# Performance work log

Measured on AMD Instinct MI355X. Metric: run time of the kernel, lower is better.

The kernel has to match this reference:

```python
import jax, jax.numpy as jnp
import numpy as np

B, D = 256, 1024
EPS = 1e-6


def setup_inputs() -> dict:
    key = jax.random.key(0)
    ks = jax.random.split(key, 8)
    s = 1.0 / np.sqrt(D)
    return {
        "x": jax.random.normal(ks[0], (B, D), jnp.float32),
        "Wq": jax.random.normal(ks[1], (D, D), jnp.float32) * s,
        "bq": jax.random.normal(ks[2], (D,), jnp.float32) * 0.01,
        "Wk": jax.random.normal(ks[3], (D, D), jnp.float32) * s,
        "bk": jax.random.normal(ks[4], (D,), jnp.float32) * 0.01,
        "Wv": jax.random.normal(ks[5], (D, D), jnp.float32) * s,
        "bv": jax.random.normal(ks[6], (D,), jnp.float32) * 0.01,
        "scale": jnp.asarray(1.0, jnp.float32),
        "norm_w": jnp.ones((D,), jnp.float32),
    }


def reference(x, Wq, bq, Wk, bk, Wv, bv, scale, norm_w):
    # QKV projections (torch Linear: x @ W.T + b)
    Q = x @ Wq.T + bq  # [B, D]
    K = x @ Wk.T + bk  # [B, D]
    V = x @ Wv.T + bv  # [B, D]
    # outer-product scores [B, D, D]: scores[b,i,j] = Q[b,i]*K[b,j]/scale
    scores = (Q[:, :, None] * K[:, None, :]) / scale
    attn = jax.nn.softmax(scores, axis=-1)  # [B, D, D]
    attended = jnp.einsum("bij,bj->bi", attn, V)  # [B, D]
    # dropout is identity in eval mode
    h = attended + x
    rms = jnp.sqrt(jnp.mean(h * h, axis=-1, keepdims=True) + EPS)
    return (h / rms) * norm_w
```

## Files before the change

kernel.cpp:

```cpp
#include <hip/hip_runtime.h>
#include <hip/hip_bf16.h>

#define BB 256
#define DD 1024

typedef unsigned short u16;
typedef unsigned int   u32;
typedef __attribute__((ext_vector_type(8))) __bf16 bf16x8;
typedef __attribute__((ext_vector_type(4))) float  floatx4;

__device__ __forceinline__ float bf2f(u16 u) {
    union { u32 i; float f; } t; t.i = ((u32)u) << 16; return t.f;
}
__device__ __forceinline__ u16 f2bf_rne(float f) {
    u32 u = __float_as_uint(f);
    u32 r = u + 0x7FFFu + ((u >> 16) & 1u);
    return (u16)(r >> 16);
}
__device__ __forceinline__ bool detect_bf16(const void* p) {
    return (*(const u32*)p) == 0x3F803F80u;
}
__device__ __forceinline__ float loadf(const void* p, int i, bool bf) {
    return bf ? bf2f(((const u16*)p)[i]) : ((const float*)p)[i];
}

__device__ __forceinline__ float wave_sum64(float x) {
    x += __int_as_float(__builtin_amdgcn_update_dpp(0, __float_as_int(x), 0x111, 0xF, 0xF, true));
    x += __int_as_float(__builtin_amdgcn_update_dpp(0, __float_as_int(x), 0x112, 0xF, 0xF, true));
    x += __int_as_float(__builtin_amdgcn_update_dpp(0, __float_as_int(x), 0x114, 0xF, 0xF, true));
    x += __int_as_float(__builtin_amdgcn_update_dpp(0, __float_as_int(x), 0x118, 0xF, 0xF, true));
    x += __int_as_float(__builtin_amdgcn_update_dpp(0, __float_as_int(x), 0x142, 0xA, 0xF, true));
    x += __int_as_float(__builtin_amdgcn_update_dpp(0, __float_as_int(x), 0x143, 0xC, 0xF, true));
    return x;
}

__device__ __forceinline__ void split1(float f, u16& h, u16& l) {
    u32 u  = __float_as_uint(f);
    u32 hu = u & 0xFFFF0000u;
    h = (u16)(hu >> 16);
    l = f2bf_rne(f - __uint_as_float(hu));
}

__global__ __launch_bounds__(256) void qkv_gemm(
    const void* __restrict__ x,
    const void* __restrict__ Wq, const void* __restrict__ bq,
    const void* __restrict__ Wk, const void* __restrict__ bk,
    const void* __restrict__ Wv, const void* __restrict__ bv,
    const void* __restrict__ nw,
    float* __restrict__ qkv)
{
    const bool bf = detect_bf16(nw);
    const int z = blockIdx.z;
    const void* W    = (z == 0) ? Wq : (z == 1) ? Wk : Wv;
    const void* bias = (z == 0) ? bq : (z == 1) ? bk : bv;
    float* outp = qkv + (size_t)z * BB * DD;

    const int m0 = blockIdx.x * 32;
    const int n0 = blockIdx.y * 64;
    const int tid  = threadIdx.x;
    const int lane = tid & 63;
    const int wave = tid >> 6;
    const int wr = wave & 1, wc = wave >> 1;
    const int l15 = lane & 15, quad = lane >> 4;

    __shared__ __align__(16) u16 Ah[32][72], Al[32][72];
    __shared__ __align__(16) u16 Bh[64][72], Bl[64][72];

    const int arow = tid >> 4;
    const int acol = (tid & 15) * 4;

    floatx4 acc[2] = {(floatx4){0.f,0.f,0.f,0.f}, (floatx4){0.f,0.f,0.f,0.f}};

    float4 ar[2], br[4];
    auto ld4 = [&](const void* p, int idx) -> float4 {
        if (!bf) return *(const float4*)((const float*)p + idx);
        const u16* q = (const u16*)p + idx;
        return make_float4(bf2f(q[0]), bf2f(q[1]), bf2f(q[2]), bf2f(q[3]));
    };
    auto fetch = [&](int k0) {
        #pragma unroll
        for (int f = 0; f < 2; ++f) ar[f] = ld4(x, (m0 + arow + f * 16) * DD + k0 + acol);
        #pragma unroll
        for (int f = 0; f < 4; ++f) br[f] = ld4(W, (n0 + arow + f * 16) * DD + k0 + acol);
    };

    fetch(0);
    for (int k0 = 0; k0 < DD; k0 += 64) {
        #pragma unroll
        for (int f = 0; f < 2; ++f) {
            const int r = arow + f * 16;
            ushort4 h, l;
            split1(ar[f].x, h.x, l.x); split1(ar[f].y, h.y, l.y);
            split1(ar[f].z, h.z, l.z); split1(ar[f].w, h.w, l.w);
            *(ushort4*)&Ah[r][acol] = h;
            *(ushort4*)&Al[r][acol] = l;
        }
        #pragma unroll
        for (int f = 0; f < 4; ++f) {
            const int r = arow + f * 16;
            ushort4 h, l;
            split1(br[f].x, h.x, l.x); split1(br[f].y, h.y, l.y);
            split1(br[f].z, h.z, l.z); split1(br[f].w, h.w, l.w);
            *(ushort4*)&Bh[r][acol] = h;
            *(ushort4*)&Bl[r][acol] = l;
        }
        __syncthreads();

        fetch((k0 + 64) & (DD - 1));

        #pragma unroll
        for (int kk = 0; kk < 2; ++kk) {
            const int ko = kk * 32 + quad * 8;
            const bf16x8 ah = *(const bf16x8*)&Ah[wr * 16 + l15][ko];
            const bf16x8 al = *(const bf16x8*)&Al[wr * 16 + l15][ko];
            #pragma unroll
            for (int ni = 0; ni < 2; ++ni) {
                const int brow = wc * 32 + ni * 16 + l15;
                const bf16x8 bh = *(const bf16x8*)&Bh[brow][ko];
                const bf16x8 bl = *(const bf16x8*)&Bl[brow][ko];
                acc[ni] = __builtin_amdgcn_mfma_f32_16x16x32_bf16(al, bh, acc[ni], 0, 0, 0);
                acc[ni] = __builtin_amdgcn_mfma_f32_16x16x32_bf16(ah, bl, acc[ni], 0, 0, 0);
                acc[ni] = __builtin_amdgcn_mfma_f32_16x16x32_bf16(ah, bh, acc[ni], 0, 0, 0);
            }
        }
        __syncthreads();
    }

    #pragma unroll
    for (int ni = 0; ni < 2; ++ni) {
        const int ng = n0 + wc * 32 + ni * 16 + l15;
        const float bv_ = loadf(bias, ng, bf);
        #pragma unroll
        for (int reg = 0; reg < 4; ++reg) {
            const int mg = m0 + wr * 16 + quad * 4 + reg;
            outp[mg * DD + ng] = acc[ni][reg] + bv_;
        }
    }
}

__global__ __launch_bounds__(1024) void attn_part(
    const float* __restrict__ qkv,
    const void* __restrict__ scale_p,
    const void* __restrict__ norm_w,
    float2* __restrict__ pws)
{
    const bool bf = detect_bf16(norm_w);
    const int b   = blockIdx.x;
    const int jh  = blockIdx.y;
    const int tid = threadIdx.x;
    const int iq  = tid & 255;
    const int jq  = tid >> 8;

    __shared__ __align__(16) float kk[512];
    __shared__ __align__(16) float vv[512];
    __shared__ float2 part[DD][4];

    const float* Qp = qkv + (size_t)b * DD;
    const float* Kp = Qp + (size_t)BB * DD;
    const float* Vp = Qp + 2 * (size_t)BB * DD;
    const float cvt = 1.44269504088896f / loadf(scale_p, 0, bf);

    if (tid < 512) {
        kk[tid] = Kp[jh * 512 + tid] * cvt;
        vv[tid] = Vp[jh * 512 + tid];
    }
    __syncthreads();

    const float q0 = Qp[iq], q1 = Qp[iq + 256], q2 = Qp[iq + 512], q3 = Qp[iq + 768];

    float S0 = 0.f, S1 = 0.f, S2 = 0.f, S3 = 0.f;
    float T0 = 0.f, T1 = 0.f, T2 = 0.f, T3 = 0.f;

    const floatx4* kk4 = (const floatx4*)kk;
    const floatx4* vv4 = (const floatx4*)vv;
    const int jb = jq * 32;

    #pragma unroll 4
    for (int mo = 0; mo < 32; mo += 2) {
        const floatx4 Ka = kk4[jb + mo],     Va = vv4[jb + mo];
        const floatx4 Kb = kk4[jb + mo + 1], Vb = vv4[jb + mo + 1];
        #pragma unroll
        for (int g = 0; g < 2; ++g) {
            const floatx4 K4 = g ? Kb : Ka;
            const floatx4 V4 = g ? Vb : Va;
            #pragma unroll
            for (int c = 0; c < 4; ++c) {
                const float kc = K4[c], vc = V4[c];
                float e;
                e = __builtin_amdgcn_exp2f(kc * q0); S0 += e; T0 = fmaf(e, vc, T0);
                e = __builtin_amdgcn_exp2f(kc * q1); S1 += e; T1 = fmaf(e, vc, T1);
                e = __builtin_amdgcn_exp2f(kc * q2); S2 += e; T2 = fmaf(e, vc, T2);
                e = __builtin_amdgcn_exp2f(kc * q3); S3 += e; T3 = fmaf(e, vc, T3);
            }
        }
    }

    part[iq +   0][jq] = make_float2(S0, T0);
    part[iq + 256][jq] = make_float2(S1, T1);
    part[iq + 512][jq] = make_float2(S2, T2);
    part[iq + 768][jq] = make_float2(S3, T3);
    __syncthreads();

    const float2 a0 = part[tid][0], a1 = part[tid][1];
    const float2 a2 = part[tid][2], a3 = part[tid][3];
    pws[((size_t)b * 2 + jh) * DD + tid] =
        make_float2((a0.x + a1.x) + (a2.x + a3.x),
                    (a0.y + a1.y) + (a2.y + a3.y));
}

__global__ __launch_bounds__(1024) void attn_fin(
    const float2* __restrict__ pws,
    const void* __restrict__ x,
    const void* __restrict__ norm_w,
    void* __restrict__ out)
{
    const bool bf = detect_bf16(norm_w);
    const int b   = blockIdx.x;
    const int tid = threadIdx.x;
    const int lane = tid & 63;
    const int wave = tid >> 6;

    __shared__ float wsum[16];

    const float2 p0 = pws[((size_t)b * 2 + 0) * DD + tid];
    const float2 p1 = pws[((size_t)b * 2 + 1) * DD + tid];
    const float Ssum = p0.x + p1.x;
    const float Tsum = p0.y + p1.y;

    const float x_l = loadf(x, b * DD + tid, bf);
    const float h = fmaf(Tsum, __builtin_amdgcn_rcpf(Ssum), x_l);

    const float ss = wave_sum64(h * h);
    if (lane == 63) wsum[wave] = ss;
    __syncthreads();
    float tot = 0.f;
    #pragma unroll
    for (int w = 0; w < 16; ++w) tot += wsum[w];
    const float rinv = __builtin_amdgcn_rsqf(tot * (1.0f / DD) + 1e-6f);
    const float val = h * rinv * loadf(norm_w, tid, bf);
    const size_t oi = (size_t)b * DD + tid;
    if (bf) ((u16*)out)[oi] = f2bf_rne(val);
    else    ((float*)out)[oi] = val;
}

extern "C" void kernel_launch(void* const* d_in, const int* in_sizes, int n_in,
                              void* d_out, int out_size, void* d_ws, size_t ws_size,
                              hipStream_t stream) {
    const void* x  = d_in[0];
    const void* Wq = d_in[1];
    const void* bq = d_in[2];
    const void* Wk = d_in[3];
    const void* bk = d_in[4];
    const void* Wv = d_in[5];
    const void* bv = d_in[6];
    const void* sc = d_in[7];
    const void* nw = d_in[8];

    float*  qkv = (float*)d_ws;
    float2* pws = (float2*)((char*)d_ws + 3u * BB * DD * sizeof(float));

    qkv_gemm<<<dim3(8, 16, 3), 256, 0, stream>>>(x, Wq, bq, Wk, bk, Wv, bv, nw, qkv);
    attn_part<<<dim3(BB, 2), 1024, 0, stream>>>(qkv, sc, nw, pws);
    attn_fin<<<dim3(BB), 1024, 0, stream>>>(pws, x, nw, d_out);
}
```

Baseline: 131.2 us.

## Fuse attention partial sums and RMSNorm finalize into one kernel

New measurement: 128.3 us. -2.2%, faster.

```diff
diff --git a/kernel.cpp b/kernel.cpp
--- a/kernel.cpp
+++ b/kernel.cpp
@@ -138,32 +138,33 @@
     }
 }
 
-__global__ __launch_bounds__(1024) void attn_part(
+__global__ __launch_bounds__(1024) void attn_norm(
     const float* __restrict__ qkv,
+    const void* __restrict__ x,
     const void* __restrict__ scale_p,
     const void* __restrict__ norm_w,
-    float2* __restrict__ pws)
+    void* __restrict__ out)
 {
     const bool bf = detect_bf16(norm_w);
     const int b   = blockIdx.x;
-    const int jh  = blockIdx.y;
     const int tid = threadIdx.x;
+    const int lane = tid & 63;
+    const int wave = tid >> 6;
     const int iq  = tid & 255;
     const int jq  = tid >> 8;
 
-    __shared__ __align__(16) float kk[512];
-    __shared__ __align__(16) float vv[512];
+    __shared__ __align__(16) float kk[DD];
+    __shared__ __align__(16) float vv[DD];
     __shared__ float2 part[DD][4];
+    __shared__ float wsum[16];
 
     const float* Qp = qkv + (size_t)b * DD;
     const float* Kp = Qp + (size_t)BB * DD;
     const float* Vp = Qp + 2 * (size_t)BB * DD;
     const float cvt = 1.44269504088896f / loadf(scale_p, 0, bf);
 
-    if (tid < 512) {
-        kk[tid] = Kp[jh * 512 + tid] * cvt;
-        vv[tid] = Vp[jh * 512 + tid];
-    }
+    kk[tid] = Kp[tid] * cvt;
+    vv[tid] = Vp[tid];
     __syncthreads();
 
     const float q0 = Qp[iq], q1 = Qp[iq + 256], q2 = Qp[iq + 512], q3 = Qp[iq + 768];
@@ -173,10 +174,10 @@
 
     const floatx4* kk4 = (const floatx4*)kk;
     const floatx4* vv4 = (const floatx4*)vv;
-    const int jb = jq * 32;
-
-    #pragma unroll 4
-    for (int mo = 0; mo < 32; mo += 2) {
+    const int jb = jq * 64;
+
+    #pragma unroll 2
+    for (int mo = 0; mo < 64; mo += 2) {
         const floatx4 Ka = kk4[jb + mo],     Va = vv4[jb + mo];
         const floatx4 Kb = kk4[jb + mo + 1], Vb = vv4[jb + mo + 1];
         #pragma unroll
@@ -203,29 +204,8 @@
 
     const float2 a0 = part[tid][0], a1 = part[tid][1];
     const float2 a2 = part[tid][2], a3 = part[tid][3];
-    pws[((size_t)b * 2 + jh) * DD + tid] =
-        make_float2((a0.x + a1.x) + (a2.x + a3.x),
-                    (a0.y + a1.y) + (a2.y + a3.y));
-}
-
-__global__ __launch_bounds__(1024) void attn_fin(
-    const float2* __restrict__ pws,
-    const void* __restrict__ x,
-    const void* __restrict__ norm_w,
-    void* __restrict__ out)
-{
-    const bool bf = detect_bf16(norm_w);
-    const int b   = blockIdx.x;
-    const int tid = threadIdx.x;
-    const int lane = tid & 63;
-    const int wave = tid >> 6;
-
-    __shared__ float wsum[16];
-
-    const float2 p0 = pws[((size_t)b * 2 + 0) * DD + tid];
-    const float2 p1 = pws[((size_t)b * 2 + 1) * DD + tid];
-    const float Ssum = p0.x + p1.x;
-    const float Tsum = p0.y + p1.y;
+    const float Ssum = (a0.x + a1.x) + (a2.x + a3.x);
+    const float Tsum = (a0.y + a1.y) + (a2.y + a3.y);
 
     const float x_l = loadf(x, b * DD + tid, bf);
     const float h = fmaf(Tsum, __builtin_amdgcn_rcpf(Ssum), x_l);
@@ -256,10 +236,8 @@
     const void* sc = d_in[7];
     const void* nw = d_in[8];
 
-    float*  qkv = (float*)d_ws;
-    float2* pws = (float2*)((char*)d_ws + 3u * BB * DD * sizeof(float));
+    float* qkv = (float*)d_ws;
 
     qkv_gemm<<<dim3(8, 16, 3), 256, 0, stream>>>(x, Wq, bq, Wk, bk, Wv, bv, nw, qkv);
-    attn_part<<<dim3(BB, 2), 1024, 0, stream>>>(qkv, sc, nw, pws);
-    attn_fin<<<dim3(BB), 1024, 0, stream>>>(pws, x, nw, d_out);
-}
+    attn_norm<<<dim3(BB), 1024, 0, stream>>>(qkv, x, sc, nw, d_out);
+}
```
